# Performance work log

Hardware: AMD Instinct MI355X
Metric: run time of the kernel (lower is better)

Reference implementation:

```python
import jax, jax.numpy as jnp
import numpy as np

LAMDA = 1.0  # init arg: weight on uniformity term
ALIGN_ALPHA = 2.0
UNIF_T = 2.0
EPS = 1e-12


def _l2_normalize(x):
    # F.normalize(x, dim=1): x / max(||x||, eps)
    n = jnp.sqrt(jnp.sum(x * x, axis=1, keepdims=True))
    return x / jnp.maximum(n, EPS)


def _lalign(q, k):
    # mean over batch of ||q_i - k_i||_2 ^ alpha (alpha=2 -> squared distance)
    d2 = jnp.sum((q - k) ** 2, axis=1)
    return jnp.mean(d2)


def _lunif(x):
    # log( mean_{i<j} exp(-t * ||x_i - x_j||^2) )
    # x is unit-norm, so ||x_i - x_j||^2 = 2 - 2 <x_i, x_j>
    n = x.shape[0]
    sq = jnp.maximum(2.0 - 2.0 * (x @ x.T), 0.0)            # [N, N] squared dists
    iu = jnp.triu(jnp.ones((n, n), dtype=bool), k=1)        # strict upper: i < j pairs
    vals = jnp.where(iu, jnp.exp(-UNIF_T * sq), 0.0)
    npairs = jnp.asarray(n * (n - 1) // 2, dtype=x.dtype)
    return jnp.log(vals.sum() / npairs)


def setup_inputs() -> dict:
    key = jax.random.key(0)
    kq, kk = jax.random.split(key)
    q = jax.random.normal(kq, (8192, 128), dtype=jnp.float32)
    k = jax.random.normal(kk, (8192, 128), dtype=jnp.float32)
    return {"q": q, "k": k}


def reference(q, k):
    qn = _l2_normalize(q)
    kn = _l2_normalize(k)
    align = _lalign(qn, kn)
    uniform = (_lunif(qn) + _lunif(kn)) / 2.0
    return align + LAMDA * uniform
```

## Files before the change

### kernel.cpp

```cpp
#include <hip/hip_runtime.h>
#include <math.h>

#define NROWS 8192
#define DIM   128
#define NT    64
#define TRI   2080

typedef __attribute__((ext_vector_type(8))) __bf16 bf16x8;
typedef __attribute__((ext_vector_type(4))) float  f32x4;
typedef __attribute__((ext_vector_type(2))) float  f32x2;

__device__ __forceinline__ unsigned short f2bf(float f) {
    unsigned int u = __float_as_uint(f);
    u += 0x7fffu + ((u >> 16) & 1u);
    return (unsigned short)(u >> 16);
}

__device__ __forceinline__ void gload_lds16(const uint4* g, uint4* l) {
    __builtin_amdgcn_global_load_lds(
        (const __attribute__((address_space(1))) uint32_t*)
            (const __attribute__((address_space(1))) void*)g,
        (__attribute__((address_space(3))) uint32_t*)
            (__attribute__((address_space(3))) void*)l,
        16, 0, 0);
}

__global__ __launch_bounds__(256) void norm_kernel(
        const float* __restrict__ q, const float* __restrict__ k,
        unsigned int* __restrict__ qn, unsigned int* __restrict__ kn,
        float* __restrict__ align_part) {
    int wave = threadIdx.x >> 6;
    int lane = threadIdx.x & 63;
    int row  = blockIdx.x * 4 + wave;

    const float2 qv = reinterpret_cast<const float2*>(q)[row * 64 + lane];
    const float2 kv = reinterpret_cast<const float2*>(k)[row * 64 + lane];

    float sq = qv.x * qv.x + qv.y * qv.y;
    float sk = kv.x * kv.x + kv.y * kv.y;
    #pragma unroll
    for (int off = 32; off; off >>= 1) {
        sq += __shfl_xor(sq, off);
        sk += __shfl_xor(sk, off);
    }
    float qi = 1.0f / fmaxf(sqrtf(sq), 1e-12f);
    float ki = 1.0f / fmaxf(sqrtf(sk), 1e-12f);
    float qx = qv.x * qi, qy = qv.y * qi;
    float kx = kv.x * ki, ky = kv.y * ki;

    qn[row * 64 + lane] = (unsigned int)f2bf(qx) | ((unsigned int)f2bf(qy) << 16);
    kn[row * 64 + lane] = (unsigned int)f2bf(kx) | ((unsigned int)f2bf(ky) << 16);

    float dx = qx - kx, dy = qy - ky;
    float d2 = dx * dx + dy * dy;
    #pragma unroll
    for (int off = 32; off; off >>= 1) d2 += __shfl_xor(d2, off);

    __shared__ float red[4];
    if (lane == 0) red[wave] = d2;
    __syncthreads();
    if (threadIdx.x == 0)
        align_part[blockIdx.x] = red[0] + red[1] + red[2] + red[3];
}

__global__ __launch_bounds__(256) void gram_kernel(
        const uint4* __restrict__ qn, const uint4* __restrict__ kn,
        float* __restrict__ unif_part) {
    __shared__ uint4 lds[4096];
    __shared__ float red[4];

    int bid = blockIdx.x;
    int mat = 0, t = bid;
    if (t >= TRI) { mat = 1; t -= TRI; }
    int ti = 0, rem = t;
    while (rem >= NT - ti) { rem -= NT - ti; ++ti; }
    int tj = ti + rem;
    const uint4* __restrict__ x = mat ? kn : qn;

    int tid = threadIdx.x;
    int wid = tid >> 6, lane = tid & 63;

    {
        int lrow4 = lane >> 4;
        int sw    = lane & 15;
        #pragma unroll
        for (int it = 0; it < 16; ++it) {
            int inst = wid * 16 + it;
            int r    = inst * 4 + lrow4;
            int rr   = r & 127;
            int tile = (r < 128) ? ti : tj;
            int s    = sw ^ (rr & 15);
            gload_lds16(&x[((size_t)tile * 128 + rr) * 16 + s], &lds[inst * 64]);
        }
    }
    __syncthreads();

    int wr = wid >> 1, wc = wid & 1;
    int lr = lane & 15, lg = lane >> 4;

    f32x4 c[4][4];
    #pragma unroll
    for (int m = 0; m < 4; ++m)
        #pragma unroll
        for (int n = 0; n < 4; ++n)
            c[m][n] = (f32x4){0.f, 0.f, 0.f, 0.f};

    #pragma unroll
    for (int ks = 0; ks < 4; ++ks) {
        int slot = ks * 4 + lg;
        bf16x8 a[4], b[4];
        #pragma unroll
        for (int m = 0; m < 4; ++m) {
            int r = wr * 64 + m * 16 + lr;
            a[m] = *reinterpret_cast<const bf16x8*>(&lds[r * 16 + (slot ^ (r & 15))]);
        }
        #pragma unroll
        for (int n = 0; n < 4; ++n) {
            int r = wc * 64 + n * 16 + lr;
            b[n] = *reinterpret_cast<const bf16x8*>(&lds[2048 + r * 16 + (slot ^ (r & 15))]);
        }
        #pragma unroll
        for (int m = 0; m < 4; ++m)
            #pragma unroll
            for (int n = 0; n < 4; ++n)
                c[m][n] = __builtin_amdgcn_mfma_f32_16x16x32_bf16(a[m], b[n], c[m][n], 0, 0, 0);
    }

    const float K1 = 4.0f * 1.4426950408889634f * 8388608.0f;
    const float B  = 1065353216.0f - 0.05744f * 8388608.0f;
    const float K0 = B - K1;
    bool diag = (ti == tj);
    float psum = 0.0f;
    if (!diag) {
        f32x2 acc2 = (f32x2){0.f, 0.f};
        #pragma unroll
        for (int m = 0; m < 4; ++m)
            #pragma unroll
            for (int n = 0; n < 4; ++n) {
                f32x4 g = c[m][n];
                f32x2 u0 = (f32x2){g[0], g[1]} * K1 + K0;
                f32x2 u1 = (f32x2){g[2], g[3]} * K1 + K0;
                f32x2 e0 = (f32x2){__int_as_float((int)u0.x),
                                   __int_as_float((int)u0.y)};
                f32x2 e1 = (f32x2){__int_as_float((int)u1.x),
                                   __int_as_float((int)u1.y)};
                acc2 += e0;
                acc2 += e1;
            }
        psum = acc2.x + acc2.y;
    } else {
        int crow0 = wr * 64 + lg * 4;
        int ccol0 = wc * 64 + lr;
        #pragma unroll
        for (int m = 0; m < 4; ++m)
            #pragma unroll
            for (int n = 0; n < 4; ++n)
                #pragma unroll
                for (int r = 0; r < 4; ++r) {
                    float u = fminf(fmaf(c[m][n][r], K1, K0), B);
                    float e = __int_as_float((int)u);
                    int lrow = crow0 + m * 16 + r;
                    int lcol = ccol0 + n * 16;
                    psum += (lcol > lrow) ? e : 0.0f;
                }
    }
    #pragma unroll
    for (int off = 32; off; off >>= 1) psum += __shfl_xor(psum, off);

    if (lane == 0) red[wid] = psum;
    __syncthreads();
    if (tid == 0)
        unif_part[bid] = red[0] + red[1] + red[2] + red[3];
}

__global__ __launch_bounds__(256) void finalize(
        const float* __restrict__ align_part,
        const float* __restrict__ unif_part,
        float* __restrict__ out) {
    int tid = threadIdx.x;
    double a = 0.0, qs = 0.0, ks = 0.0;
    for (int i = tid; i < 2048; i += 256) a  += (double)align_part[i];
    for (int i = tid; i < TRI;  i += 256) qs += (double)unif_part[i];
    for (int i = tid; i < TRI;  i += 256) ks += (double)unif_part[TRI + i];

    __shared__ double sa[256], sq[256], sk[256];
    sa[tid] = a; sq[tid] = qs; sk[tid] = ks;
    __syncthreads();
    for (int s = 128; s; s >>= 1) {
        if (tid < s) {
            sa[tid] += sa[tid + s];
            sq[tid] += sq[tid + s];
            sk[tid] += sk[tid + s];
        }
        __syncthreads();
    }
    if (tid == 0) {
        const double npairs = (double)NROWS * (NROWS - 1) / 2.0;
        double align = sa[0] / (double)NROWS;
        double lq = log(sq[0] / npairs);
        double lk = log(sk[0] / npairs);
        out[0] = (float)(align + 0.5 * (lq + lk));
    }
}

extern "C" void kernel_launch(void* const* d_in, const int* in_sizes, int n_in,
                              void* d_out, int out_size, void* d_ws, size_t ws_size,
                              hipStream_t stream) {
    const float* q = (const float*)d_in[0];
    const float* k = (const float*)d_in[1];
    char* ws = (char*)d_ws;
    unsigned int* qn = (unsigned int*)ws;
    unsigned int* kn = (unsigned int*)(ws + (size_t)2 * 1024 * 1024);
    float* align_part = (float*)(ws + (size_t)4 * 1024 * 1024);
    float* unif_part  = (float*)(ws + (size_t)4 * 1024 * 1024 + 16384);
    float* out = (float*)d_out;

    norm_kernel<<<NROWS / 4, 256, 0, stream>>>(q, k, qn, kn, align_part);
    gram_kernel<<<2 * TRI, 256, 0, stream>>>((const uint4*)qn, (const uint4*)kn, unif_part);
    finalize<<<1, 256, 0, stream>>>(align_part, unif_part, out);
}
```

Measured before the change: 103.2 us.

## Make gram kernel persistent over tile chunks with register prefetch of next tile

Each gram block now processes a chunk of eight tile pairs instead of one. While the current tile's MFMA and exp-sum run, the next tile is loaded from global memory into registers. Direct global-to-LDS loads are replaced by register staging with swizzled LDS stores, and separate q/k partial sums are kept. The aim is to hide load latency and reduce launch and tail cost, at the price of 520 blocks (around two per CU), higher register pressure and less occupancy for hiding latency.

```diff
diff --git a/kernel.cpp b/kernel.cpp
--- a/kernel.cpp
+++ b/kernel.cpp
@@ -5,6 +5,8 @@
 #define DIM   128
 #define NT    64
 #define TRI   2080
+#define CHUNK 8
+#define NBLK  520
 
 typedef __attribute__((ext_vector_type(8))) __bf16 bf16x8;
 typedef __attribute__((ext_vector_type(4))) float  f32x4;
@@ -16,13 +18,12 @@
     return (unsigned short)(u >> 16);
 }
 
-__device__ __forceinline__ void gload_lds16(const uint4* g, uint4* l) {
-    __builtin_amdgcn_global_load_lds(
-        (const __attribute__((address_space(1))) uint32_t*)
-            (const __attribute__((address_space(1))) void*)g,
-        (__attribute__((address_space(3))) uint32_t*)
-            (__attribute__((address_space(3))) void*)l,
-        16, 0, 0);
+__device__ __forceinline__ void decode_tile(int t, int& mat, int& ti, int& tj) {
+    mat = 0;
+    if (t >= TRI) { mat = 1; t -= TRI; }
+    int i = 0;
+    while (t >= NT - i) { t -= NT - i; ++i; }
+    ti = i; tj = i + t;
 }
 
 __global__ __launch_bounds__(256) void norm_kernel(
@@ -65,123 +66,151 @@
 
 __global__ __launch_bounds__(256) void gram_kernel(
         const uint4* __restrict__ qn, const uint4* __restrict__ kn,
-        float* __restrict__ unif_part) {
+        float* __restrict__ unif_q, float* __restrict__ unif_k) {
     __shared__ uint4 lds[4096];
-    __shared__ float red[4];
-
-    int bid = blockIdx.x;
-    int mat = 0, t = bid;
-    if (t >= TRI) { mat = 1; t -= TRI; }
-    int ti = 0, rem = t;
-    while (rem >= NT - ti) { rem -= NT - ti; ++ti; }
-    int tj = ti + rem;
-    const uint4* __restrict__ x = mat ? kn : qn;
+    __shared__ float redq[4], redk[4];
 
     int tid = threadIdx.x;
     int wid = tid >> 6, lane = tid & 63;
-
-    {
-        int lrow4 = lane >> 4;
-        int sw    = lane & 15;
-        #pragma unroll
-        for (int it = 0; it < 16; ++it) {
-            int inst = wid * 16 + it;
-            int r    = inst * 4 + lrow4;
-            int rr   = r & 127;
-            int tile = (r < 128) ? ti : tj;
-            int s    = sw ^ (rr & 15);
-            gload_lds16(&x[((size_t)tile * 128 + rr) * 16 + s], &lds[inst * 64]);
-        }
-    }
-    __syncthreads();
-
     int wr = wid >> 1, wc = wid & 1;
     int lr = lane & 15, lg = lane >> 4;
-
-    f32x4 c[4][4];
-    #pragma unroll
-    for (int m = 0; m < 4; ++m)
-        #pragma unroll
-        for (int n = 0; n < 4; ++n)
-            c[m][n] = (f32x4){0.f, 0.f, 0.f, 0.f};
-
-    #pragma unroll
-    for (int ks = 0; ks < 4; ++ks) {
-        int slot = ks * 4 + lg;
-        bf16x8 a[4], b[4];
-        #pragma unroll
-        for (int m = 0; m < 4; ++m) {
-            int r = wr * 64 + m * 16 + lr;
-            a[m] = *reinterpret_cast<const bf16x8*>(&lds[r * 16 + (slot ^ (r & 15))]);
-        }
-        #pragma unroll
-        for (int n = 0; n < 4; ++n) {
-            int r = wc * 64 + n * 16 + lr;
-            b[n] = *reinterpret_cast<const bf16x8*>(&lds[2048 + r * 16 + (slot ^ (r & 15))]);
-        }
-        #pragma unroll
-        for (int m = 0; m < 4; ++m)
-            #pragma unroll
-            for (int n = 0; n < 4; ++n)
-                c[m][n] = __builtin_amdgcn_mfma_f32_16x16x32_bf16(a[m], b[n], c[m][n], 0, 0, 0);
-    }
 
     const float K1 = 4.0f * 1.4426950408889634f * 8388608.0f;
     const float B  = 1065353216.0f - 0.05744f * 8388608.0f;
     const float K0 = B - K1;
-    bool diag = (ti == tj);
-    float psum = 0.0f;
-    if (!diag) {
-        f32x2 acc2 = (f32x2){0.f, 0.f};
+
+    int t0 = blockIdx.x * CHUNK;
+
+    uint4 pre[16];
+    int nmat, nti, ntj;
+    decode_tile(t0, nmat, nti, ntj);
+    {
+        const uint4* __restrict__ x = nmat ? kn : qn;
+        #pragma unroll
+        for (int i = 0; i < 16; ++i) {
+            int li = i * 256 + tid;
+            int rr = li >> 4, s = li & 15;
+            int r7 = rr & 127;
+            int tl = (rr < 128) ? nti : ntj;
+            pre[i] = x[((size_t)tl * 128 + r7) * 16 + s];
+        }
+    }
+
+    f32x2 aq2 = (f32x2){0.f, 0.f}, ak2 = (f32x2){0.f, 0.f};
+
+    for (int u = 0; u < CHUNK; ++u) {
+        #pragma unroll
+        for (int i = 0; i < 16; ++i) {
+            int li = i * 256 + tid;
+            int rr = li >> 4, s = li & 15;
+            lds[rr * 16 + (s ^ (rr & 15))] = pre[i];
+        }
+        __syncthreads();
+
+        int dmat = nmat, dti = nti, dtj = ntj;
+
+        if (u + 1 < CHUNK) {
+            decode_tile(t0 + u + 1, nmat, nti, ntj);
+            const uint4* __restrict__ x = nmat ? kn : qn;
+            #pragma unroll
+            for (int i = 0; i < 16; ++i) {
+                int li = i * 256 + tid;
+                int rr = li >> 4, s = li & 15;
+                int r7 = rr & 127;
+                int tl = (rr < 128) ? nti : ntj;
+                pre[i] = x[((size_t)tl * 128 + r7) * 16 + s];
+            }
+        }
+
+        f32x4 c[4][4];
         #pragma unroll
         for (int m = 0; m < 4; ++m)
             #pragma unroll
+            for (int n = 0; n < 4; ++n)
+                c[m][n] = (f32x4){0.f, 0.f, 0.f, 0.f};
+
+        #pragma unroll
+        for (int ks = 0; ks < 4; ++ks) {
+            int slot = ks * 4 + lg;
+            bf16x8 a[4], b[4];
+            #pragma unroll
+            for (int m = 0; m < 4; ++m) {
+                int r = wr * 64 + m * 16 + lr;
+                a[m] = *reinterpret_cast<const bf16x8*>(&lds[r * 16 + (slot ^ (r & 15))]);
+            }
+            #pragma unroll
             for (int n = 0; n < 4; ++n) {
-                f32x4 g = c[m][n];
-                f32x2 u0 = (f32x2){g[0], g[1]} * K1 + K0;
-                f32x2 u1 = (f32x2){g[2], g[3]} * K1 + K0;
-                f32x2 e0 = (f32x2){__int_as_float((int)u0.x),
-                                   __int_as_float((int)u0.y)};
-                f32x2 e1 = (f32x2){__int_as_float((int)u1.x),
-                                   __int_as_float((int)u1.y)};
-                acc2 += e0;
-                acc2 += e1;
+                int r = wc * 64 + n * 16 + lr;
+                b[n] = *reinterpret_cast<const bf16x8*>(&lds[2048 + r * 16 + (slot ^ (r & 15))]);
             }
-        psum = acc2.x + acc2.y;
-    } else {
-        int crow0 = wr * 64 + lg * 4;
-        int ccol0 = wc * 64 + lr;
-        #pragma unroll
-        for (int m = 0; m < 4; ++m)
-            #pragma unroll
-            for (int n = 0; n < 4; ++n)
+            #pragma unroll
+            for (int m = 0; m < 4; ++m)
                 #pragma unroll
-                for (int r = 0; r < 4; ++r) {
-                    float u = fminf(fmaf(c[m][n][r], K1, K0), B);
-                    float e = __int_as_float((int)u);
-                    int lrow = crow0 + m * 16 + r;
-                    int lcol = ccol0 + n * 16;
-                    psum += (lcol > lrow) ? e : 0.0f;
+                for (int n = 0; n < 4; ++n)
+                    c[m][n] = __builtin_amdgcn_mfma_f32_16x16x32_bf16(a[m], b[n], c[m][n], 0, 0, 0);
+        }
+
+        f32x2 p2 = (f32x2){0.f, 0.f};
+        if (dti != dtj) {
+            #pragma unroll
+            for (int m = 0; m < 4; ++m)
+                #pragma unroll
+                for (int n = 0; n < 4; ++n) {
+                    f32x4 g = c[m][n];
+                    f32x2 u0 = (f32x2){g[0], g[1]} * K1 + K0;
+                    f32x2 u1 = (f32x2){g[2], g[3]} * K1 + K0;
+                    p2 += (f32x2){__int_as_float((int)u0.x),
+                                  __int_as_float((int)u0.y)};
+                    p2 += (f32x2){__int_as_float((int)u1.x),
+                                  __int_as_float((int)u1.y)};
                 }
-    }
+        } else {
+            int crow0 = wr * 64 + lg * 4;
+            int ccol0 = wc * 64 + lr;
+            float ps = 0.0f;
+            #pragma unroll
+            for (int m = 0; m < 4; ++m)
+                #pragma unroll
+                for (int n = 0; n < 4; ++n)
+                    #pragma unroll
+                    for (int r = 0; r < 4; ++r) {
+                        float uu = fminf(fmaf(c[m][n][r], K1, K0), B);
+                        float e = __int_as_float((int)uu);
+                        int lrow = crow0 + m * 16 + r;
+                        int lcol = ccol0 + n * 16;
+                        ps += (lcol > lrow) ? e : 0.0f;
+                    }
+            p2.x = ps;
+        }
+        if (dmat) ak2 += p2; else aq2 += p2;
+
+        __syncthreads();
+    }
+
+    float pq = aq2.x + aq2.y, pk = ak2.x + ak2.y;
     #pragma unroll
-    for (int off = 32; off; off >>= 1) psum += __shfl_xor(psum, off);
-
-    if (lane == 0) red[wid] = psum;
+    for (int off = 32; off; off >>= 1) {
+        pq += __shfl_xor(pq, off);
+        pk += __shfl_xor(pk, off);
+    }
+    if (lane == 0) { redq[wid] = pq; redk[wid] = pk; }
     __syncthreads();
-    if (tid == 0)
-        unif_part[bid] = red[0] + red[1] + red[2] + red[3];
+    if (tid == 0) {
+        unif_q[blockIdx.x] = redq[0] + redq[1] + redq[2] + redq[3];
+        unif_k[blockIdx.x] = redk[0] + redk[1] + redk[2] + redk[3];
+    }
 }
 
 __global__ __launch_bounds__(256) void finalize(
         const float* __restrict__ align_part,
-        const float* __restrict__ unif_part,
+        const float* __restrict__ unif_q,
+        const float* __restrict__ unif_k,
         float* __restrict__ out) {
     int tid = threadIdx.x;
     double a = 0.0, qs = 0.0, ks = 0.0;
     for (int i = tid; i < 2048; i += 256) a  += (double)align_part[i];
-    for (int i = tid; i < TRI;  i += 256) qs += (double)unif_part[i];
-    for (int i = tid; i < TRI;  i += 256) ks += (double)unif_part[TRI + i];
+    for (int i = tid; i < NBLK; i += 256) qs += (double)unif_q[i];
+    for (int i = tid; i < NBLK; i += 256) ks += (double)unif_k[i];
 
     __shared__ double sa[256], sq[256], sk[256];
     sa[tid] = a; sq[tid] = qs; sk[tid] = ks;
@@ -212,10 +241,11 @@
     unsigned int* qn = (unsigned int*)ws;
     unsigned int* kn = (unsigned int*)(ws + (size_t)2 * 1024 * 1024);
     float* align_part = (float*)(ws + (size_t)4 * 1024 * 1024);
-    float* unif_part  = (float*)(ws + (size_t)4 * 1024 * 1024 + 16384);
+    float* unif_q = (float*)(ws + (size_t)4 * 1024 * 1024 + 16384);
+    float* unif_k = (float*)(ws + (size_t)4 * 1024 * 1024 + 32768);
     float* out = (float*)d_out;
 
     norm_kernel<<<NROWS / 4, 256, 0, stream>>>(q, k, qn, kn, align_part);
-    gram_kernel<<<2 * TRI, 256, 0, stream>>>((const uint4*)qn, (const uint4*)kn, unif_part);
-    finalize<<<1, 256, 0, stream>>>(align_part, unif_part, out);
-}
+    gram_kernel<<<NBLK, 256, 0, stream>>>((const uint4*)qn, (const uint4*)kn, unif_q, unif_k);
+    finalize<<<1, 256, 0, stream>>>(align_part, unif_q, unif_k, out);
+}
```

After: 209.5 us. +103.1%, slower.
